# Performance work log

Hardware: AMD Instinct MI355X
Metric: run time of the kernel (lower is better)

Reference implementation:

```python
import jax, jax.numpy as jnp
import numpy as np
import math

K_BRANCH = 8  # config['k']

def _selectors(n, k):
    # Static (trace-time) construction of per-level gather indices, mask=True branch.
    L = math.ceil(math.log(n) / math.log(k)) + 1
    rel = [0] + [math.ceil(n / k ** i) for i in range(L)]  # level sizes, leaves first
    Li = np.cumsum(np.array(rel))                          # level start offsets in node dim
    sels = []
    for l in range(L):
        m = rel[l + 1]
        i = np.arange(m)[:, None]
        anc = None
        if l < L - 1:
            m_next = rel[l + 2]
            j = np.arange(m_next)[None, :]
            cond = (j + 1) / m_next <= i / m
            anc = np.where(cond, Li[l + 1] + j, 0)
        s = np.arange(k)[None, :]
        ridx = np.minimum(i // k * k + s, m - 1)
        sib = np.where(ridx <= i, Li[l] + ridx, 0)  # rel/m <= i/m  <=>  rel <= i
        chi = None
        if l >= 1:
            m_prev = rel[l]
            c = np.arange(k)[None, :]
            ridx = np.minimum(i * k + c, m_prev - 1)
            cond = ridx / m_prev <= i / m
            chi = np.where(cond, Li[l - 1] + ridx, 0)
        sels.append((anc, sib, chi))
    return L, Li, sels

def _sdp(q, Kmat, Vmat, sel, d):
    keys = Kmat[:, :, sel, :]   # [b,h,m,w,d] gather
    vals = Vmat[:, :, sel, :]
    logits = jnp.einsum('bhnd,bhnkd->bhnk', q, keys) / math.sqrt(d)
    w = jax.nn.softmax(logits, axis=-1)
    return jnp.einsum('bhnk,bhnkd->bhnd', w, vals)

def setup_inputs() -> dict:
    key = jax.random.key(0)
    k1, k2, k3 = jax.random.split(key, 3)
    b, h, n_tot, d = 2, 4, 585, 128
    return {
        'Q': jax.random.normal(k1, (b, h, n_tot, d), dtype=jnp.float32),
        'K': jax.random.normal(k2, (b, h, n_tot, d), dtype=jnp.float32),
        'V': jax.random.normal(k3, (b, h, n_tot, d), dtype=jnp.float32),
        'n': 512,
    }

def reference(Q, K, V, n):
    k = K_BRANCH
    d = Q.shape[-1]
    L, Li, sels = _selectors(int(n), k)
    # Sequential bottom-up level updates: V at level l is rewritten before level l+1 reads it.
    for l in range(L):
        anc, sib, chi = sels[l]
        q = Q[:, :, Li[l]:Li[l + 1], :]
        out = _sdp(q, K, V, sib, d)
        if anc is not None:
            out = out + _sdp(q, K, V, anc, d)
        if chi is not None:
            out = out + _sdp(q, K, V, chi, d)
        V = V.at[:, :, Li[l]:Li[l + 1], :].set(out / 3.0)
    return V
```

## Files before the change

kernel.cpp:

```cpp
#include <hip/hip_runtime.h>
#include <math.h>

#define D 128
#define NTOT 585
#define SCALE 0.08838834764831845f
#define THIRD 0.33333333333333333f
#define LROW 132

__device__ __forceinline__ float rsum_c(float v) {
    v += __shfl_xor(v, 1, 64);
    v += __shfl_xor(v, 2, 64);
    v += __shfl_xor(v, 4, 64);
    return v;
}
__device__ __forceinline__ float rsum_s(float v) {
    v += __shfl_xor(v, 8, 64);
    v += __shfl_xor(v, 16, 64);
    v += __shfl_xor(v, 32, 64);
    return v;
}
__device__ __forceinline__ float rmax_s(float v) {
    v = fmaxf(v, __shfl_xor(v, 8, 64));
    v = fmaxf(v, __shfl_xor(v, 16, 64));
    v = fmaxf(v, __shfl_xor(v, 32, 64));
    return v;
}
__device__ __forceinline__ float dot16(const float4 q[4], const float* __restrict__ row, int c) {
    const float4* k = (const float4*)(row + (c << 4));
    float4 k0 = k[0], k1 = k[1], k2 = k[2], k3 = k[3];
    float p0 = q[0].x * k0.x + q[0].y * k0.y + q[0].z * k0.z + q[0].w * k0.w;
    float p1 = q[1].x * k1.x + q[1].y * k1.y + q[1].z * k1.z + q[1].w * k1.w;
    float p2 = q[2].x * k2.x + q[2].y * k2.y + q[2].z * k2.z + q[2].w * k2.w;
    float p3 = q[3].x * k3.x + q[3].y * k3.y + q[3].z * k3.z + q[3].w * k3.w;
    return (p0 + p1) + (p2 + p3);
}
__device__ __forceinline__ void vacc(float w, const float* __restrict__ row, int c, float4 acc[4]) {
    const float4* v = (const float4*)(row + (c << 4));
#pragma unroll
    for (int u = 0; u < 4; ++u) {
        float4 t = v[u];
        acc[u].x += w * t.x; acc[u].y += w * t.y; acc[u].z += w * t.z; acc[u].w += w * t.w;
    }
}
__device__ __forceinline__ void vacc_reg(float w, const float4 vv[4], float4 acc[4]) {
#pragma unroll
    for (int u = 0; u < 4; ++u) {
        acc[u].x += w * vv[u].x; acc[u].y += w * vv[u].y;
        acc[u].z += w * vv[u].z; acc[u].w += w * vv[u].w;
    }
}
__device__ __forceinline__ void loadq(const float* __restrict__ qrow, int c, float4 q[4]) {
    const float4* qp = (const float4*)(qrow + (c << 4));
#pragma unroll
    for (int u = 0; u < 4; ++u) q[u] = qp[u];
}
__device__ __forceinline__ void butterfly_acc(float4 acc[4]) {
#pragma unroll
    for (int u = 0; u < 4; ++u) {
        acc[u].x = rsum_s(acc[u].x);
        acc[u].y = rsum_s(acc[u].y);
        acc[u].z = rsum_s(acc[u].z);
        acc[u].w = rsum_s(acc[u].w);
    }
}

__global__ __launch_bounds__(1024) void level0_lds(const float* __restrict__ Q,
                                                   const float* __restrict__ K,
                                                   const float* __restrict__ V,
                                                   float* __restrict__ Out) {
    __shared__ float Ks[81 * LROW];
    __shared__ float Vs[81 * LROW];
    const int tid = threadIdx.x;
    const int lane = tid & 63;
    const int s = lane >> 3, c = lane & 7;
    const int bh = blockIdx.x >> 5;
    const int qb0 = (blockIdx.x & 31) << 4;
    const float* Qb = Q + (size_t)bh * NTOT * D;
    const float* Kb = K + (size_t)bh * NTOT * D;
    const float* Vb = V + (size_t)bh * NTOT * D;
    float* Ob = Out + (size_t)bh * NTOT * D;

    for (int t = tid; t < 81 * 32; t += 1024) {
        const int row = t >> 5, col = (t & 31) << 2;
        const int src = (row < 16) ? (qb0 + row) : ((row < 80) ? (512 + row - 16) : 0);
        *(float4*)(&Ks[row * LROW + col]) = *(const float4*)(Kb + (size_t)src * D + col);
        *(float4*)(&Vs[row * LROW + col]) = *(const float4*)(Vb + (size_t)src * D + col);
    }
    __syncthreads();

    const int w = tid >> 6;
    const int i = qb0 + w;
    const int sl = i & 7;
    const int g = i >> 3;
    const int sibbase = w & 8;

    float4 q4[4];
    loadq(Qb + (size_t)i * D, c, q4);
    float4 acc[4] = {{0,0,0,0},{0,0,0,0},{0,0,0,0},{0,0,0,0}};
    const float lg0 = rsum_c(dot16(q4, &Ks[80 * LROW], c)) * SCALE;

    {
        float lg = -1e30f;
        if (s <= sl)
            lg = rsum_c(dot16(q4, &Ks[(sibbase + s) * LROW], c)) * SCALE;
        const float m = fmaxf(rmax_s(lg), lg0);
        const float e = (s <= sl) ? __expf(lg - m) : 0.f;
        const float e0 = __expf(lg0 - m);
        float zp = e;
        if (s == 0) zp += (float)(7 - sl) * e0;
        const float inv = 1.f / rsum_s(zp);
        if (s <= sl) vacc(e * inv, &Vs[(sibbase + s) * LROW], c, acc);
        if (s == 0 && sl < 7) vacc((float)(7 - sl) * e0 * inv, &Vs[80 * LROW], c, acc);
    }

    {
        float lgA[8];
        float mloc = lg0;
#pragma unroll
        for (int R = 0; R < 4; ++R) {
            if (16 * R < g) {
#pragma unroll
                for (int rr = 0; rr < 2; ++rr) {
                    const int r = 2 * R + rr;
                    const int j = 8 * r + s;
                    float lg = -1e30f;
                    if (j < g)
                        lg = rsum_c(dot16(q4, &Ks[(16 + j) * LROW], c)) * SCALE;
                    lgA[r] = lg;
                    mloc = fmaxf(mloc, lg);
                }
            } else { lgA[2 * R] = -1e30f; lgA[2 * R + 1] = -1e30f; }
        }
        const float m = rmax_s(mloc);
        const float e0 = __expf(lg0 - m);
        float zp = (s == 0) ? (float)(64 - g) * e0 : 0.f;
        float eA[8];
#pragma unroll
        for (int R = 0; R < 4; ++R) {
            if (16 * R < g) {
#pragma unroll
                for (int rr = 0; rr < 2; ++rr) {
                    const int r = 2 * R + rr;
                    eA[r] = (lgA[r] > -1e29f) ? __expf(lgA[r] - m) : 0.f;
                    zp += eA[r];
                }
            }
        }
        const float inv = 1.f / rsum_s(zp);
#pragma unroll
        for (int R = 0; R < 4; ++R) {
            if (16 * R < g) {
#pragma unroll
                for (int rr = 0; rr < 2; ++rr) {
                    const int r = 2 * R + rr;
                    const int j = 8 * r + s;
                    if (j < g) vacc(eA[r] * inv, &Vs[(16 + j) * LROW], c, acc);
                }
            }
        }
        if (s == 0) vacc((float)(64 - g) * e0 * inv, &Vs[80 * LROW], c, acc);
    }
    butterfly_acc(acc);
    if (s == 0) {
        float4* orow = (float4*)(Ob + (size_t)i * D + (c << 4));
#pragma unroll
        for (int u = 0; u < 4; ++u)
            orow[u] = make_float4(acc[u].x * THIRD, acc[u].y * THIRD,
                                  acc[u].z * THIRD, acc[u].w * THIRD);
    }
}

__global__ __launch_bounds__(512) void level123_lds(const float* __restrict__ Q,
                                                    const float* __restrict__ K,
                                                    const float* __restrict__ V,
                                                    float* __restrict__ Out) {
    __shared__ float Ks[17 * LROW];
    __shared__ float Vs[17 * LROW];
    const int tid = threadIdx.x;
    const int lane = tid & 63;
    const int s = lane >> 3, c = lane & 7;
    const int bh = blockIdx.x >> 3;
    const int gq = blockIdx.x & 7;
    const float* Qb = Q + (size_t)bh * NTOT * D;
    const float* Kb = K + (size_t)bh * NTOT * D;
    const float* Vb = V + (size_t)bh * NTOT * D;
    float* Ob = Out + (size_t)bh * NTOT * D;

    for (int t = tid; t < 17 * 32; t += 512) {
        const int row = t >> 5, col = (t & 31) << 2;
        const int src = (row < 8) ? (512 + 8 * gq + row) : ((row < 16) ? (576 + row - 8) : 0);
        *(float4*)(&Ks[row * LROW + col]) = *(const float4*)(Kb + (size_t)src * D + col);
        *(float4*)(&Vs[row * LROW + col]) = *(const float4*)(Vb + (size_t)src * D + col);
    }
    __syncthreads();

    const int w = tid >> 6;
    const int i = 8 * gq + w;

    float4 v0n[4];
    {
        const float4* vp = (const float4*)(&Vs[16 * LROW] + (c << 4));
#pragma unroll
        for (int u = 0; u < 4; ++u) {
            float4 v = vp[u];
            v0n[u] = make_float4(v.x * (2.f * THIRD), v.y * (2.f * THIRD),
                                 v.z * (2.f * THIRD), v.w * (2.f * THIRD));
        }
    }
    float4 o0[4];
    if (i == 0) {
#pragma unroll
        for (int u = 0; u < 4; ++u) o0[u] = v0n[u];
    } else {
        const float4* op = (const float4*)(Ob + (size_t)(8 * i) * D + (c << 4));
#pragma unroll
        for (int u = 0; u < 4; ++u) o0[u] = op[u];
    }

    float4 o1[4];
    {
        float4 q1[4];
        loadq(Qb + (size_t)(512 + i) * D, c, q1);
        float4 acc[4] = {{0,0,0,0},{0,0,0,0},{0,0,0,0},{0,0,0,0}};
        const float lg0q = rsum_c(dot16(q1, &Ks[16 * LROW], c)) * SCALE;
        const int sl1 = w;
        {
            float lg = -1e30f;
            if (s <= sl1)
                lg = rsum_c(dot16(q1, &Ks[s * LROW], c)) * SCALE;
            const float m = fmaxf(rmax_s(lg), lg0q);
            const float e = (s <= sl1) ? __expf(lg - m) : 0.f;
            const float e0 = __expf(lg0q - m);
            float zp = e;
            if (s == 0) zp += (float)(7 - sl1) * e0;
            const float inv = 1.f / rsum_s(zp);
            if (s <= sl1) vacc(e * inv, &Vs[s * LROW], c, acc);
            if (s == 0 && sl1 < 7) vacc_reg((float)(7 - sl1) * e0 * inv, v0n, acc);
        }
        {
            float lg = -1e30f;
            if (s < gq)
                lg = rsum_c(dot16(q1, &Ks[(8 + s) * LROW], c)) * SCALE;
            const float m = fmaxf(rmax_s(lg), lg0q);
            const float e = (s < gq) ? __expf(lg - m) : 0.f;
            const float e0 = __expf(lg0q - m);
            float zp = e;
            if (s == 0) zp += (float)(8 - gq) * e0;
            const float inv = 1.f / rsum_s(zp);
            if (s < gq) vacc(e * inv, &Vs[(8 + s) * LROW], c, acc);
            if (s == 0) vacc_reg((float)(8 - gq) * e0 * inv, v0n, acc);
        }
        {
            float lg = -1e30f;
            if (s == 0)
                lg = rsum_c(dot16(q1, Kb + (size_t)(8 * i) * D, c)) * SCALE;
            const float m = fmaxf(rmax_s(lg), lg0q);
            const float e = (s == 0) ? __expf(lg - m) : 0.f;
            const float e0 = __expf(lg0q - m);
            const float zp = (s == 0) ? (e + 7.f * e0) : 0.f;
            const float inv = 1.f / rsum_s(zp);
            if (s == 0) {
                vacc_reg(e * inv, o0, acc);
                vacc_reg(7.f * e0 * inv, v0n, acc);
            }
        }
        butterfly_acc(acc);
#pragma unroll
        for (int u = 0; u < 4; ++u)
            o1[u] = make_float4(acc[u].x * THIRD, acc[u].y * THIRD,
                                acc[u].z * THIRD, acc[u].w * THIRD);
        if (s == 0) {
            float4* orow = (float4*)(Ob + (size_t)(512 + i) * D + (c << 4));
#pragma unroll
            for (int u = 0; u < 4; ++u) orow[u] = o1[u];
        }
    }

    if (w == 0) {
        const int j = gq;
        float4 q2[4];
        loadq(Qb + (size_t)(576 + j) * D, c, q2);
        float4 acc[4] = {{0,0,0,0},{0,0,0,0},{0,0,0,0},{0,0,0,0}};
        const float lg0q = rsum_c(dot16(q2, &Ks[16 * LROW], c)) * SCALE;
        {
            float lg = -1e30f;
            if (s <= j)
                lg = rsum_c(dot16(q2, &Ks[(8 + s) * LROW], c)) * SCALE;
            const float m = fmaxf(rmax_s(lg), lg0q);
            const float e = (s <= j) ? __expf(lg - m) : 0.f;
            const float e0 = __expf(lg0q - m);
            float zp = e;
            if (s == 0) zp += (float)(7 - j) * e0;
            const float inv = 1.f / rsum_s(zp);
            if (s <= j) vacc(e * inv, &Vs[(8 + s) * LROW], c, acc);
            if (s == 0 && j < 7) vacc_reg((float)(7 - j) * e0 * inv, v0n, acc);
        }
        {
            float lg = -1e30f;
            if (s == 0)
                lg = rsum_c(dot16(q2, &Ks[0], c)) * SCALE;
            const float m = fmaxf(rmax_s(lg), lg0q);
            const float e = (s == 0) ? __expf(lg - m) : 0.f;
            const float e0 = __expf(lg0q - m);
            const float zp = (s == 0) ? (e + 7.f * e0) : 0.f;
            const float inv = 1.f / rsum_s(zp);
            if (s == 0) {
                vacc_reg(e * inv, o1, acc);
                vacc_reg(7.f * e0 * inv, v0n, acc);
            }
        }
        butterfly_acc(acc);
        float4 o2[4];
#pragma unroll
        for (int u = 0; u < 4; ++u)
            o2[u] = make_float4((acc[u].x + v0n[u].x) * THIRD, (acc[u].y + v0n[u].y) * THIRD,
                                (acc[u].z + v0n[u].z) * THIRD, (acc[u].w + v0n[u].w) * THIRD);
        if (s == 0) {
            float4* orow = (float4*)(Ob + (size_t)(576 + j) * D + (c << 4));
#pragma unroll
            for (int u = 0; u < 4; ++u) orow[u] = o2[u];
        }

        if (j == 0) {
            float4 q3[4];
            loadq(Qb + (size_t)584 * D, c, q3);
            const float lg0r = rsum_c(dot16(q3, &Ks[16 * LROW], c)) * SCALE;
            float lg = -1e30f;
            if (s == 0)
                lg = rsum_c(dot16(q3, &Ks[8 * LROW], c)) * SCALE;
            const float m = fmaxf(rmax_s(lg), lg0r);
            const float e = (s == 0) ? __expf(lg - m) : 0.f;
            const float e0 = __expf(lg0r - m);
            const float zp = (s == 0) ? (e + 7.f * e0) : 0.f;
            const float inv = 1.f / rsum_s(zp);
            float4 acc3[4] = {{0,0,0,0},{0,0,0,0},{0,0,0,0},{0,0,0,0}};
            if (s == 0) {
                vacc_reg(e * inv, o2, acc3);
                vacc_reg(7.f * e0 * inv, v0n, acc3);
            }
            butterfly_acc(acc3);
            if (s == 0) {
                const float4* v584 = (const float4*)(Vb + (size_t)584 * D + (c << 4));
                float4* orow = (float4*)(Ob + (size_t)584 * D + (c << 4));
#pragma unroll
                for (int u = 0; u < 4; ++u) {
                    float4 bb = v584[u];
                    orow[u] = make_float4((acc3[u].x + bb.x) * THIRD,
                                          (acc3[u].y + bb.y) * THIRD,
                                          (acc3[u].z + bb.z) * THIRD,
                                          (acc3[u].w + bb.w) * THIRD);
                }
            }
        }
    }
}

extern "C" void kernel_launch(void* const* d_in, const int* in_sizes, int n_in,
                              void* d_out, int out_size, void* d_ws, size_t ws_size,
                              hipStream_t stream) {
    const float* Q = (const float*)d_in[0];
    const float* K = (const float*)d_in[1];
    const float* V = (const float*)d_in[2];
    float* Out = (float*)d_out;
    hipLaunchKernelGGL(level0_lds, dim3(256), dim3(1024), 0, stream, Q, K, V, Out);
    hipLaunchKernelGGL(level123_lds, dim3(64), dim3(512), 0, stream, Q, K, V, Out);
}
```

Measured before the change: 79.54 us.

## Fuse level-0 and upper-level kernels into one launch with recomputation

Merges the two kernels into a single launch. Each block now also handles the level-1, level-2 and level-3 nodes whose children it owns. The level-0 outputs needed by upper levels are recomputed in registers instead of being read back from global memory, and the extra level-2 K/V rows are staged in shared memory. This removes the second kernel launch and the inter-kernel dependency, at the cost of redundant level-0 work and a longer tail on the first waves of each block.

```diff
diff --git a/kernel.cpp b/kernel.cpp
--- a/kernel.cpp
+++ b/kernel.cpp
@@ -64,12 +64,63 @@
     }
 }
 
-__global__ __launch_bounds__(1024) void level0_lds(const float* __restrict__ Q,
-                                                   const float* __restrict__ K,
-                                                   const float* __restrict__ V,
-                                                   float* __restrict__ Out) {
-    __shared__ float Ks[81 * LROW];
-    __shared__ float Vs[81 * LROW];
+__device__ __forceinline__ void anc_l0(const float4 q4[4], int g, int s, int c,
+                                       const float* __restrict__ Ks,
+                                       const float* __restrict__ Vs,
+                                       float lg0, float4 acc[4]) {
+    float lgA[8];
+    float mloc = lg0;
+#pragma unroll
+    for (int R = 0; R < 4; ++R) {
+        if (16 * R < g) {
+#pragma unroll
+            for (int rr = 0; rr < 2; ++rr) {
+                const int r = 2 * R + rr;
+                const int j = 8 * r + s;
+                float lg = -1e30f;
+                if (j < g)
+                    lg = rsum_c(dot16(q4, &Ks[(16 + j) * LROW], c)) * SCALE;
+                lgA[r] = lg;
+                mloc = fmaxf(mloc, lg);
+            }
+        } else { lgA[2 * R] = -1e30f; lgA[2 * R + 1] = -1e30f; }
+    }
+    const float m = rmax_s(mloc);
+    const float e0 = __expf(lg0 - m);
+    float zp = (s == 0) ? (float)(64 - g) * e0 : 0.f;
+    float eA[8];
+#pragma unroll
+    for (int R = 0; R < 4; ++R) {
+        if (16 * R < g) {
+#pragma unroll
+            for (int rr = 0; rr < 2; ++rr) {
+                const int r = 2 * R + rr;
+                eA[r] = (lgA[r] > -1e29f) ? __expf(lgA[r] - m) : 0.f;
+                zp += eA[r];
+            }
+        }
+    }
+    const float inv = 1.f / rsum_s(zp);
+#pragma unroll
+    for (int R = 0; R < 4; ++R) {
+        if (16 * R < g) {
+#pragma unroll
+            for (int rr = 0; rr < 2; ++rr) {
+                const int r = 2 * R + rr;
+                const int j = 8 * r + s;
+                if (j < g) vacc(eA[r] * inv, &Vs[(16 + j) * LROW], c, acc);
+            }
+        }
+    }
+    if (s == 0) vacc((float)(64 - g) * e0 * inv, &Vs[80 * LROW], c, acc);
+}
+
+__global__ __launch_bounds__(1024) void sequoia_fused(const float* __restrict__ Q,
+                                                      const float* __restrict__ K,
+                                                      const float* __restrict__ V,
+                                                      float* __restrict__ Out) {
+    __shared__ float Ks[89 * LROW];
+    __shared__ float Vs[89 * LROW];
     const int tid = threadIdx.x;
     const int lane = tid & 63;
     const int s = lane >> 3, c = lane & 7;
@@ -80,275 +131,237 @@
     const float* Vb = V + (size_t)bh * NTOT * D;
     float* Ob = Out + (size_t)bh * NTOT * D;
 
-    for (int t = tid; t < 81 * 32; t += 1024) {
+    for (int t = tid; t < 89 * 32; t += 1024) {
         const int row = t >> 5, col = (t & 31) << 2;
-        const int src = (row < 16) ? (qb0 + row) : ((row < 80) ? (512 + row - 16) : 0);
+        int src;
+        if (row < 16)      src = qb0 + row;
+        else if (row < 80) src = 512 + row - 16;
+        else if (row == 80) src = 0;
+        else               src = 576 + (row - 81);
         *(float4*)(&Ks[row * LROW + col]) = *(const float4*)(Kb + (size_t)src * D + col);
         *(float4*)(&Vs[row * LROW + col]) = *(const float4*)(Vb + (size_t)src * D + col);
     }
     __syncthreads();
 
     const int w = tid >> 6;
-    const int i = qb0 + w;
-    const int sl = i & 7;
-    const int g = i >> 3;
-    const int sibbase = w & 8;
-
-    float4 q4[4];
-    loadq(Qb + (size_t)i * D, c, q4);
-    float4 acc[4] = {{0,0,0,0},{0,0,0,0},{0,0,0,0},{0,0,0,0}};
-    const float lg0 = rsum_c(dot16(q4, &Ks[80 * LROW], c)) * SCALE;
 
     {
-        float lg = -1e30f;
-        if (s <= sl)
-            lg = rsum_c(dot16(q4, &Ks[(sibbase + s) * LROW], c)) * SCALE;
-        const float m = fmaxf(rmax_s(lg), lg0);
-        const float e = (s <= sl) ? __expf(lg - m) : 0.f;
-        const float e0 = __expf(lg0 - m);
-        float zp = e;
-        if (s == 0) zp += (float)(7 - sl) * e0;
-        const float inv = 1.f / rsum_s(zp);
-        if (s <= sl) vacc(e * inv, &Vs[(sibbase + s) * LROW], c, acc);
-        if (s == 0 && sl < 7) vacc((float)(7 - sl) * e0 * inv, &Vs[80 * LROW], c, acc);
-    }
-
-    {
-        float lgA[8];
-        float mloc = lg0;
-#pragma unroll
-        for (int R = 0; R < 4; ++R) {
-            if (16 * R < g) {
-#pragma unroll
-                for (int rr = 0; rr < 2; ++rr) {
-                    const int r = 2 * R + rr;
-                    const int j = 8 * r + s;
-                    float lg = -1e30f;
-                    if (j < g)
-                        lg = rsum_c(dot16(q4, &Ks[(16 + j) * LROW], c)) * SCALE;
-                    lgA[r] = lg;
-                    mloc = fmaxf(mloc, lg);
-                }
-            } else { lgA[2 * R] = -1e30f; lgA[2 * R + 1] = -1e30f; }
-        }
-        const float m = rmax_s(mloc);
-        const float e0 = __expf(lg0 - m);
-        float zp = (s == 0) ? (float)(64 - g) * e0 : 0.f;
-        float eA[8];
-#pragma unroll
-        for (int R = 0; R < 4; ++R) {
-            if (16 * R < g) {
-#pragma unroll
-                for (int rr = 0; rr < 2; ++rr) {
-                    const int r = 2 * R + rr;
-                    eA[r] = (lgA[r] > -1e29f) ? __expf(lgA[r] - m) : 0.f;
-                    zp += eA[r];
-                }
-            }
-        }
-        const float inv = 1.f / rsum_s(zp);
-#pragma unroll
-        for (int R = 0; R < 4; ++R) {
-            if (16 * R < g) {
-#pragma unroll
-                for (int rr = 0; rr < 2; ++rr) {
-                    const int r = 2 * R + rr;
-                    const int j = 8 * r + s;
-                    if (j < g) vacc(eA[r] * inv, &Vs[(16 + j) * LROW], c, acc);
-                }
-            }
-        }
-        if (s == 0) vacc((float)(64 - g) * e0 * inv, &Vs[80 * LROW], c, acc);
-    }
-    butterfly_acc(acc);
-    if (s == 0) {
-        float4* orow = (float4*)(Ob + (size_t)i * D + (c << 4));
-#pragma unroll
-        for (int u = 0; u < 4; ++u)
-            orow[u] = make_float4(acc[u].x * THIRD, acc[u].y * THIRD,
-                                  acc[u].z * THIRD, acc[u].w * THIRD);
-    }
-}
-
-__global__ __launch_bounds__(512) void level123_lds(const float* __restrict__ Q,
-                                                    const float* __restrict__ K,
-                                                    const float* __restrict__ V,
-                                                    float* __restrict__ Out) {
-    __shared__ float Ks[17 * LROW];
-    __shared__ float Vs[17 * LROW];
-    const int tid = threadIdx.x;
-    const int lane = tid & 63;
-    const int s = lane >> 3, c = lane & 7;
-    const int bh = blockIdx.x >> 3;
-    const int gq = blockIdx.x & 7;
-    const float* Qb = Q + (size_t)bh * NTOT * D;
-    const float* Kb = K + (size_t)bh * NTOT * D;
-    const float* Vb = V + (size_t)bh * NTOT * D;
-    float* Ob = Out + (size_t)bh * NTOT * D;
-
-    for (int t = tid; t < 17 * 32; t += 512) {
-        const int row = t >> 5, col = (t & 31) << 2;
-        const int src = (row < 8) ? (512 + 8 * gq + row) : ((row < 16) ? (576 + row - 8) : 0);
-        *(float4*)(&Ks[row * LROW + col]) = *(const float4*)(Kb + (size_t)src * D + col);
-        *(float4*)(&Vs[row * LROW + col]) = *(const float4*)(Vb + (size_t)src * D + col);
-    }
-    __syncthreads();
-
-    const int w = tid >> 6;
-    const int i = 8 * gq + w;
-
-    float4 v0n[4];
-    {
-        const float4* vp = (const float4*)(&Vs[16 * LROW] + (c << 4));
-#pragma unroll
-        for (int u = 0; u < 4; ++u) {
-            float4 v = vp[u];
-            v0n[u] = make_float4(v.x * (2.f * THIRD), v.y * (2.f * THIRD),
-                                 v.z * (2.f * THIRD), v.w * (2.f * THIRD));
-        }
-    }
-    float4 o0[4];
-    if (i == 0) {
-#pragma unroll
-        for (int u = 0; u < 4; ++u) o0[u] = v0n[u];
-    } else {
-        const float4* op = (const float4*)(Ob + (size_t)(8 * i) * D + (c << 4));
-#pragma unroll
-        for (int u = 0; u < 4; ++u) o0[u] = op[u];
-    }
-
-    float4 o1[4];
-    {
-        float4 q1[4];
-        loadq(Qb + (size_t)(512 + i) * D, c, q1);
+        const int i = qb0 + w;
+        const int sl = i & 7;
+        const int g = i >> 3;
+        const int sibbase = w & 8;
+
+        float4 q4[4];
+        loadq(Qb + (size_t)i * D, c, q4);
         float4 acc[4] = {{0,0,0,0},{0,0,0,0},{0,0,0,0},{0,0,0,0}};
-        const float lg0q = rsum_c(dot16(q1, &Ks[16 * LROW], c)) * SCALE;
-        const int sl1 = w;
+        const float lg0 = rsum_c(dot16(q4, &Ks[80 * LROW], c)) * SCALE;
         {
             float lg = -1e30f;
-            if (s <= sl1)
-                lg = rsum_c(dot16(q1, &Ks[s * LROW], c)) * SCALE;
-            const float m = fmaxf(rmax_s(lg), lg0q);
-            const float e = (s <= sl1) ? __expf(lg - m) : 0.f;
-            const float e0 = __expf(lg0q - m);
+            if (s <= sl)
+                lg = rsum_c(dot16(q4, &Ks[(sibbase + s) * LROW], c)) * SCALE;
+            const float m = fmaxf(rmax_s(lg), lg0);
+            const float e = (s <= sl) ? __expf(lg - m) : 0.f;
+            const float e0 = __expf(lg0 - m);
             float zp = e;
-            if (s == 0) zp += (float)(7 - sl1) * e0;
+            if (s == 0) zp += (float)(7 - sl) * e0;
             const float inv = 1.f / rsum_s(zp);
-            if (s <= sl1) vacc(e * inv, &Vs[s * LROW], c, acc);
-            if (s == 0 && sl1 < 7) vacc_reg((float)(7 - sl1) * e0 * inv, v0n, acc);
-        }
+            if (s <= sl) vacc(e * inv, &Vs[(sibbase + s) * LROW], c, acc);
+            if (s == 0 && sl < 7) vacc((float)(7 - sl) * e0 * inv, &Vs[80 * LROW], c, acc);
+        }
+        anc_l0(q4, g, s, c, Ks, Vs, lg0, acc);
+        butterfly_acc(acc);
+        if (s == 0) {
+            float4* orow = (float4*)(Ob + (size_t)i * D + (c << 4));
+#pragma unroll
+            for (int u = 0; u < 4; ++u)
+                orow[u] = make_float4(acc[u].x * THIRD, acc[u].y * THIRD,
+                                      acc[u].z * THIRD, acc[u].w * THIRD);
+        }
+    }
+
+    if (w < 2) {
+        const int ci = (qb0 >> 3) + w;
+
+        float4 v0n[4];
         {
-            float lg = -1e30f;
-            if (s < gq)
-                lg = rsum_c(dot16(q1, &Ks[(8 + s) * LROW], c)) * SCALE;
-            const float m = fmaxf(rmax_s(lg), lg0q);
-            const float e = (s < gq) ? __expf(lg - m) : 0.f;
-            const float e0 = __expf(lg0q - m);
-            float zp = e;
-            if (s == 0) zp += (float)(8 - gq) * e0;
-            const float inv = 1.f / rsum_s(zp);
-            if (s < gq) vacc(e * inv, &Vs[(8 + s) * LROW], c, acc);
-            if (s == 0) vacc_reg((float)(8 - gq) * e0 * inv, v0n, acc);
-        }
+            const float4* vp = (const float4*)(&Vs[80 * LROW] + (c << 4));
+#pragma unroll
+            for (int u = 0; u < 4; ++u) {
+                float4 v = vp[u];
+                v0n[u] = make_float4(v.x * (2.f * THIRD), v.y * (2.f * THIRD),
+                                     v.z * (2.f * THIRD), v.w * (2.f * THIRD));
+            }
+        }
+
+        float4 o0[4];
+        if (ci == 0) {
+#pragma unroll
+            for (int u = 0; u < 4; ++u) o0[u] = v0n[u];
+        } else {
+            float4 q0[4];
+            loadq(Qb + (size_t)(8 * ci) * D, c, q0);
+            float4 acc[4] = {{0,0,0,0},{0,0,0,0},{0,0,0,0},{0,0,0,0}};
+            const float lg0 = rsum_c(dot16(q0, &Ks[80 * LROW], c)) * SCALE;
+            {
+                float lg = -1e30f;
+                if (s == 0)
+                    lg = rsum_c(dot16(q0, &Ks[(8 * w) * LROW], c)) * SCALE;
+                const float m = fmaxf(rmax_s(lg), lg0);
+                const float e = (s == 0) ? __expf(lg - m) : 0.f;
+                const float e0 = __expf(lg0 - m);
+                float zp = e;
+                if (s == 0) zp += 7.f * e0;
+                const float inv = 1.f / rsum_s(zp);
+                if (s == 0) {
+                    vacc(e * inv, &Vs[(8 * w) * LROW], c, acc);
+                    vacc(7.f * e0 * inv, &Vs[80 * LROW], c, acc);
+                }
+            }
+            anc_l0(q0, ci, s, c, Ks, Vs, lg0, acc);
+            butterfly_acc(acc);
+#pragma unroll
+            for (int u = 0; u < 4; ++u)
+                o0[u] = make_float4(acc[u].x * THIRD, acc[u].y * THIRD,
+                                    acc[u].z * THIRD, acc[u].w * THIRD);
+        }
+
+        float4 o1[4];
         {
-            float lg = -1e30f;
-            if (s == 0)
-                lg = rsum_c(dot16(q1, Kb + (size_t)(8 * i) * D, c)) * SCALE;
-            const float m = fmaxf(rmax_s(lg), lg0q);
-            const float e = (s == 0) ? __expf(lg - m) : 0.f;
-            const float e0 = __expf(lg0q - m);
-            const float zp = (s == 0) ? (e + 7.f * e0) : 0.f;
-            const float inv = 1.f / rsum_s(zp);
+            float4 q1[4];
+            loadq(Qb + (size_t)(512 + ci) * D, c, q1);
+            float4 acc[4] = {{0,0,0,0},{0,0,0,0},{0,0,0,0},{0,0,0,0}};
+            const float lg0q = rsum_c(dot16(q1, &Ks[80 * LROW], c)) * SCALE;
+            const int sl1 = ci & 7;
+            const int gq = ci >> 3;
+            {
+                const int slot = 16 + (ci & ~7) + s;
+                float lg = -1e30f;
+                if (s <= sl1)
+                    lg = rsum_c(dot16(q1, &Ks[slot * LROW], c)) * SCALE;
+                const float m = fmaxf(rmax_s(lg), lg0q);
+                const float e = (s <= sl1) ? __expf(lg - m) : 0.f;
+                const float e0 = __expf(lg0q - m);
+                float zp = e;
+                if (s == 0) zp += (float)(7 - sl1) * e0;
+                const float inv = 1.f / rsum_s(zp);
+                if (s <= sl1) vacc(e * inv, &Vs[slot * LROW], c, acc);
+                if (s == 0 && sl1 < 7) vacc_reg((float)(7 - sl1) * e0 * inv, v0n, acc);
+            }
+            {
+                float lg = -1e30f;
+                if (s < gq)
+                    lg = rsum_c(dot16(q1, &Ks[(81 + s) * LROW], c)) * SCALE;
+                const float m = fmaxf(rmax_s(lg), lg0q);
+                const float e = (s < gq) ? __expf(lg - m) : 0.f;
+                const float e0 = __expf(lg0q - m);
+                float zp = e;
+                if (s == 0) zp += (float)(8 - gq) * e0;
+                const float inv = 1.f / rsum_s(zp);
+                if (s < gq) vacc(e * inv, &Vs[(81 + s) * LROW], c, acc);
+                if (s == 0) vacc_reg((float)(8 - gq) * e0 * inv, v0n, acc);
+            }
+            {
+                float lg = -1e30f;
+                if (s == 0)
+                    lg = rsum_c(dot16(q1, &Ks[(8 * w) * LROW], c)) * SCALE;
+                const float m = fmaxf(rmax_s(lg), lg0q);
+                const float e = (s == 0) ? __expf(lg - m) : 0.f;
+                const float e0 = __expf(lg0q - m);
+                const float zp = (s == 0) ? (e + 7.f * e0) : 0.f;
+                const float inv = 1.f / rsum_s(zp);
+                if (s == 0) {
+                    vacc_reg(e * inv, o0, acc);
+                    vacc_reg(7.f * e0 * inv, v0n, acc);
+                }
+            }
+            butterfly_acc(acc);
+#pragma unroll
+            for (int u = 0; u < 4; ++u)
+                o1[u] = make_float4(acc[u].x * THIRD, acc[u].y * THIRD,
+                                    acc[u].z * THIRD, acc[u].w * THIRD);
             if (s == 0) {
-                vacc_reg(e * inv, o0, acc);
-                vacc_reg(7.f * e0 * inv, v0n, acc);
-            }
-        }
-        butterfly_acc(acc);
-#pragma unroll
-        for (int u = 0; u < 4; ++u)
-            o1[u] = make_float4(acc[u].x * THIRD, acc[u].y * THIRD,
-                                acc[u].z * THIRD, acc[u].w * THIRD);
-        if (s == 0) {
-            float4* orow = (float4*)(Ob + (size_t)(512 + i) * D + (c << 4));
-#pragma unroll
-            for (int u = 0; u < 4; ++u) orow[u] = o1[u];
-        }
-    }
-
-    if (w == 0) {
-        const int j = gq;
-        float4 q2[4];
-        loadq(Qb + (size_t)(576 + j) * D, c, q2);
-        float4 acc[4] = {{0,0,0,0},{0,0,0,0},{0,0,0,0},{0,0,0,0}};
-        const float lg0q = rsum_c(dot16(q2, &Ks[16 * LROW], c)) * SCALE;
-        {
-            float lg = -1e30f;
-            if (s <= j)
-                lg = rsum_c(dot16(q2, &Ks[(8 + s) * LROW], c)) * SCALE;
-            const float m = fmaxf(rmax_s(lg), lg0q);
-            const float e = (s <= j) ? __expf(lg - m) : 0.f;
-            const float e0 = __expf(lg0q - m);
-            float zp = e;
-            if (s == 0) zp += (float)(7 - j) * e0;
-            const float inv = 1.f / rsum_s(zp);
-            if (s <= j) vacc(e * inv, &Vs[(8 + s) * LROW], c, acc);
-            if (s == 0 && j < 7) vacc_reg((float)(7 - j) * e0 * inv, v0n, acc);
-        }
-        {
-            float lg = -1e30f;
-            if (s == 0)
-                lg = rsum_c(dot16(q2, &Ks[0], c)) * SCALE;
-            const float m = fmaxf(rmax_s(lg), lg0q);
-            const float e = (s == 0) ? __expf(lg - m) : 0.f;
-            const float e0 = __expf(lg0q - m);
-            const float zp = (s == 0) ? (e + 7.f * e0) : 0.f;
-            const float inv = 1.f / rsum_s(zp);
+                float4* orow = (float4*)(Ob + (size_t)(512 + ci) * D + (c << 4));
+#pragma unroll
+                for (int u = 0; u < 4; ++u) orow[u] = o1[u];
+            }
+        }
+
+        if (w == 0 && (ci & 7) == 0) {
+            const int j = ci >> 3;
+            float4 q2[4];
+            loadq(Qb + (size_t)(576 + j) * D, c, q2);
+            float4 acc[4] = {{0,0,0,0},{0,0,0,0},{0,0,0,0},{0,0,0,0}};
+            const float lg0q = rsum_c(dot16(q2, &Ks[80 * LROW], c)) * SCALE;
+            {
+                float lg = -1e30f;
+                if (s <= j)
+                    lg = rsum_c(dot16(q2, &Ks[(81 + s) * LROW], c)) * SCALE;
+                const float m = fmaxf(rmax_s(lg), lg0q);
+                const float e = (s <= j) ? __expf(lg - m) : 0.f;
+                const float e0 = __expf(lg0q - m);
+                float zp = e;
+                if (s == 0) zp += (float)(7 - j) * e0;
+                const float inv = 1.f / rsum_s(zp);
+                if (s <= j) vacc(e * inv, &Vs[(81 + s) * LROW], c, acc);
+                if (s == 0 && j < 7) vacc_reg((float)(7 - j) * e0 * inv, v0n, acc);
+            }
+            {
+                float lg = -1e30f;
+                if (s == 0)
+                    lg = rsum_c(dot16(q2, &Ks[(16 + 8 * j) * LROW], c)) * SCALE;
+                const float m = fmaxf(rmax_s(lg), lg0q);
+                const float e = (s == 0) ? __expf(lg - m) : 0.f;
+                const float e0 = __expf(lg0q - m);
+                const float zp = (s == 0) ? (e + 7.f * e0) : 0.f;
+                const float inv = 1.f / rsum_s(zp);
+                if (s == 0) {
+                    vacc_reg(e * inv, o1, acc);
+                    vacc_reg(7.f * e0 * inv, v0n, acc);
+                }
+            }
+            butterfly_acc(acc);
+            float4 o2[4];
+#pragma unroll
+            for (int u = 0; u < 4; ++u)
+                o2[u] = make_float4((acc[u].x + v0n[u].x) * THIRD,
+                                    (acc[u].y + v0n[u].y) * THIRD,
+                                    (acc[u].z + v0n[u].z) * THIRD,
+                                    (acc[u].w + v0n[u].w) * THIRD);
             if (s == 0) {
-                vacc_reg(e * inv, o1, acc);
-                vacc_reg(7.f * e0 * inv, v0n, acc);
-            }
-        }
-        butterfly_acc(acc);
-        float4 o2[4];
-#pragma unroll
-        for (int u = 0; u < 4; ++u)
-            o2[u] = make_float4((acc[u].x + v0n[u].x) * THIRD, (acc[u].y + v0n[u].y) * THIRD,
-                                (acc[u].z + v0n[u].z) * THIRD, (acc[u].w + v0n[u].w) * THIRD);
-        if (s == 0) {
-            float4* orow = (float4*)(Ob + (size_t)(576 + j) * D + (c << 4));
-#pragma unroll
-            for (int u = 0; u < 4; ++u) orow[u] = o2[u];
-        }
-
-        if (j == 0) {
-            float4 q3[4];
-            loadq(Qb + (size_t)584 * D, c, q3);
-            const float lg0r = rsum_c(dot16(q3, &Ks[16 * LROW], c)) * SCALE;
-            float lg = -1e30f;
-            if (s == 0)
-                lg = rsum_c(dot16(q3, &Ks[8 * LROW], c)) * SCALE;
-            const float m = fmaxf(rmax_s(lg), lg0r);
-            const float e = (s == 0) ? __expf(lg - m) : 0.f;
-            const float e0 = __expf(lg0r - m);
-            const float zp = (s == 0) ? (e + 7.f * e0) : 0.f;
-            const float inv = 1.f / rsum_s(zp);
-            float4 acc3[4] = {{0,0,0,0},{0,0,0,0},{0,0,0,0},{0,0,0,0}};
-            if (s == 0) {
-                vacc_reg(e * inv, o2, acc3);
-                vacc_reg(7.f * e0 * inv, v0n, acc3);
-            }
-            butterfly_acc(acc3);
-            if (s == 0) {
-                const float4* v584 = (const float4*)(Vb + (size_t)584 * D + (c << 4));
-                float4* orow = (float4*)(Ob + (size_t)584 * D + (c << 4));
-#pragma unroll
-                for (int u = 0; u < 4; ++u) {
-                    float4 bb = v584[u];
-                    orow[u] = make_float4((acc3[u].x + bb.x) * THIRD,
-                                          (acc3[u].y + bb.y) * THIRD,
-                                          (acc3[u].z + bb.z) * THIRD,
-                                          (acc3[u].w + bb.w) * THIRD);
+                float4* orow = (float4*)(Ob + (size_t)(576 + j) * D + (c << 4));
+#pragma unroll
+                for (int u = 0; u < 4; ++u) orow[u] = o2[u];
+            }
+
+            if (j == 0) {
+                float4 q3[4];
+                loadq(Qb + (size_t)584 * D, c, q3);
+                const float lg0r = rsum_c(dot16(q3, &Ks[80 * LROW], c)) * SCALE;
+                float lg = -1e30f;
+                if (s == 0)
+                    lg = rsum_c(dot16(q3, &Ks[81 * LROW], c)) * SCALE;
+                const float m = fmaxf(rmax_s(lg), lg0r);
+                const float e = (s == 0) ? __expf(lg - m) : 0.f;
+                const float e0 = __expf(lg0r - m);
+                const float zp = (s == 0) ? (e + 7.f * e0) : 0.f;
+                const float inv = 1.f / rsum_s(zp);
+                float4 acc3[4] = {{0,0,0,0},{0,0,0,0},{0,0,0,0},{0,0,0,0}};
+                if (s == 0) {
+                    vacc_reg(e * inv, o2, acc3);
+                    vacc_reg(7.f * e0 * inv, v0n, acc3);
+                }
+                butterfly_acc(acc3);
+                if (s == 0) {
+                    const float4* v584 = (const float4*)(Vb + (size_t)584 * D + (c << 4));
+                    float4* orow = (float4*)(Ob + (size_t)584 * D + (c << 4));
+#pragma unroll
+                    for (int u = 0; u < 4; ++u) {
+                        float4 bb = v584[u];
+                        orow[u] = make_float4((acc3[u].x + bb.x) * THIRD,
+                                              (acc3[u].y + bb.y) * THIRD,
+                                              (acc3[u].z + bb.z) * THIRD,
+                                              (acc3[u].w + bb.w) * THIRD);
+                    }
                 }
             }
         }
@@ -362,6 +375,5 @@
     const float* K = (const float*)d_in[1];
     const float* V = (const float*)d_in[2];
     float* Out = (float*)d_out;
-    hipLaunchKernelGGL(level0_lds, dim3(256), dim3(1024), 0, stream, Q, K, V, Out);
-    hipLaunchKernelGGL(level123_lds, dim3(64), dim3(512), 0, stream, Q, K, V, Out);
-}
+    hipLaunchKernelGGL(sequoia_fused, dim3(256), dim3(1024), 0, stream, Q, K, V, Out);
+}
```

After: 76.59 us. -3.7%, faster.
